# Kernel tuning notes

Hardware: AMD Instinct MI355X
Metric: run time of the kernel (lower is better)

The kernel has to match this reference:

```python
import jax, jax.numpy as jnp
import numpy as np

N_NODES = 50000
N_EDGES = 800000
IN_DIM = 128
HID = 96
ATTN_HID = 32
OUT_DIM = 16
N_SPOTS = 5000
EPS = 1e-5


def _glorot(k, shape):
    fan_in, fan_out = shape
    lim = float(np.sqrt(6.0 / (fan_in + fan_out)))
    return jax.random.uniform(k, shape, minval=-lim, maxval=lim, dtype=jnp.float32)


def setup_inputs() -> dict:
    key = jax.random.key(0)
    ks = jax.random.split(key, 16)
    f32 = jnp.float32
    inp = {
        'x': jax.random.normal(ks[0], (N_NODES, IN_DIM), dtype=f32),
        'edge_index': jax.random.randint(ks[1], (2, N_EDGES), 0, N_NODES, dtype=jnp.int32),
        'cell_to_spot': jax.random.randint(ks[2], (N_NODES,), 0, N_SPOTS, dtype=jnp.int32),
        'num_spots': N_SPOTS,
        # proj: Linear(IN_DIM, HID) + GraphNorm(HID)
        'proj_W': _glorot(ks[3], (IN_DIM, HID)), 'proj_b': jnp.zeros((HID,), f32),
        'gn0_w': jnp.ones((HID,), f32), 'gn0_b': jnp.zeros((HID,), f32), 'gn0_a': jnp.ones((HID,), f32),
        # GCN layer 1 + GraphNorm
        'gcn1_W': _glorot(ks[4], (HID, HID)), 'gcn1_b': jnp.zeros((HID,), f32),
        'gn1_w': jnp.ones((HID,), f32), 'gn1_b': jnp.zeros((HID,), f32), 'gn1_a': jnp.ones((HID,), f32),
        # GCN layer 2 + GraphNorm
        'gcn2_W': _glorot(ks[5], (HID, HID)), 'gcn2_b': jnp.zeros((HID,), f32),
        'gn2_w': jnp.ones((HID,), f32), 'gn2_b': jnp.zeros((HID,), f32), 'gn2_a': jnp.ones((HID,), f32),
        # spot attention aggregator MLP
        'attn_W1': _glorot(ks[6], (HID, ATTN_HID)), 'attn_b1': jnp.zeros((ATTN_HID,), f32),
        'attn_W2': _glorot(ks[7], (ATTN_HID, 1)), 'attn_b2': jnp.zeros((1,), f32),
        # MLP head: Linear + GraphNorm + ReLU + Linear
        'mlp_W1': _glorot(ks[8], (HID, HID)), 'mlp_b1': jnp.zeros((HID,), f32),
        'mlp_gn_w': jnp.ones((HID,), f32), 'mlp_gn_b': jnp.zeros((HID,), f32), 'mlp_gn_a': jnp.ones((HID,), f32),
        'mlp_W2': _glorot(ks[9], (HID, OUT_DIM)), 'mlp_b2': jnp.zeros((OUT_DIM,), f32),
    }
    return inp


def graph_norm(x, w, b, a):
    # PyG GraphNorm over the single graph (all nodes)
    mean = jnp.mean(x, axis=0, keepdims=True)           # [1, d]
    centered = x - a * mean                              # [n, d]
    var = jnp.mean(centered * centered, axis=0, keepdims=True)
    return w * centered * jax.lax.rsqrt(var + EPS) + b


def gcn_conv(x, W, b, src, dst, n):
    # PyG GCNConv: add self-loops, symmetric normalization
    h = x @ W                                            # [n, d_out]
    deg = jax.ops.segment_sum(jnp.ones((src.shape[0],), x.dtype), dst, num_segments=n) + 1.0
    dinv = jax.lax.rsqrt(deg)                            # deg >= 1 due to self loops
    norm = dinv[src] * dinv[dst]                         # [E]
    agg = jax.ops.segment_sum(h[src] * norm[:, None], dst, num_segments=n)
    agg = agg + (dinv * dinv)[:, None] * h               # self-loop messages
    return agg + b


def segment_softmax(scores, seg, num_segments):
    smax = jax.ops.segment_max(scores, seg, num_segments=num_segments)
    e = jnp.exp(scores - smax[seg])
    denom = jax.ops.segment_sum(e, seg, num_segments=num_segments)
    return e / denom[seg]


def reference(x, edge_index, cell_to_spot, num_spots,
              proj_W, proj_b, gn0_w, gn0_b, gn0_a,
              gcn1_W, gcn1_b, gn1_w, gn1_b, gn1_a,
              gcn2_W, gcn2_b, gn2_w, gn2_b, gn2_a,
              attn_W1, attn_b1, attn_W2, attn_b2,
              mlp_W1, mlp_b1, mlp_gn_w, mlp_gn_b, mlp_gn_a,
              mlp_W2, mlp_b2):
    n = x.shape[0]
    src, dst = edge_index[0], edge_index[1]
    # proj: Linear + GraphNorm + ReLU
    h = jax.nn.relu(graph_norm(x @ proj_W + proj_b, gn0_w, gn0_b, gn0_a))
    # GCN stack
    h = jax.nn.relu(graph_norm(gcn_conv(h, gcn1_W, gcn1_b, src, dst, n), gn1_w, gn1_b, gn1_a))
    h = jax.nn.relu(graph_norm(gcn_conv(h, gcn2_W, gcn2_b, src, dst, n), gn2_w, gn2_b, gn2_a))
    # spot attention aggregation
    scores = (jax.nn.relu(h @ attn_W1 + attn_b1) @ attn_W2 + attn_b2)[:, 0]  # [n]
    attn = segment_softmax(scores, cell_to_spot, num_spots)                  # [n]
    spot = jax.ops.segment_sum(h * attn[:, None], cell_to_spot, num_segments=num_spots)  # [S, d]
    # MLP head
    z = jax.nn.relu(graph_norm(spot @ mlp_W1 + mlp_b1, mlp_gn_w, mlp_gn_b, mlp_gn_a))
    return z @ mlp_W2 + mlp_b2
```

## Files before the change

### kernel.cpp

```cpp
#include <hip/hip_runtime.h>

#define N_NODES 50000
#define N_EDGES 800000
#define IN_DIM 128
#define HID 96
#define ATTN_HID 32
#define OUT_DIM 16
#define N_SPOTS 5000
#define GN_EPS 1e-5f

#define SCAN_NB ((N_NODES + 255) / 256)
#define SCAN_SB ((N_SPOTS + 255) / 256)
#define NXCD 8
#define NRANGE (N_NODES / NXCD)
#define SRANGE (N_SPOTS / NXCD)
#define CSB 256
#define GTHB 6250

typedef short bf16x8 __attribute__((ext_vector_type(8)));
typedef float f32x4 __attribute__((ext_vector_type(4)));

__device__ __align__(16) float g_bufA[N_NODES * HID];
__device__ __align__(16) float g_bufB[N_NODES * HID];
__device__ __align__(16) float g_bufC[N_NODES * HID];
__device__ __align__(16) float g_spot[N_SPOTS * HID];
__device__ float    g_dinv[N_NODES];
__device__ float    g_scores[N_NODES];
__device__ int      g_deg[N_NODES];
__device__ int      g_degs[N_SPOTS];
__device__ int      g_rp[N_NODES + 1];
__device__ int      g_cur[N_NODES];
__device__ int      g_rps[N_SPOTS + 1];
__device__ int      g_curs[N_SPOTS];
__device__ int      g_csrc[N_EDGES];
__device__ int      g_cnode[N_NODES];
__device__ int      g_partN[SCAN_NB];
__device__ int      g_partS[SCAN_SB];
__device__ float    g_gpart[GTHB][2 * HID];
__device__ float    g_Spart[CSB][2 * HID];
__device__ float    g_ab[4 * 2 * HID];

__device__ __forceinline__ float* pick(int id) {
  switch (id) {
    case 0:  return g_bufA;
    case 1:  return g_bufB;
    case 2:  return g_bufC;
    default: return g_spot;
  }
}

__device__ __forceinline__ unsigned short bf16_rn(float f) {
  unsigned u = __float_as_uint(f);
  unsigned r = u + 0x7FFFu + ((u >> 16) & 1u);
  return (unsigned short)(r >> 16);
}

__global__ __launch_bounds__(256) void k_init() {
  int i = blockIdx.x * 256 + threadIdx.x;
  if (i < N_NODES) g_deg[i] = 0;
  if (i < N_SPOTS) g_degs[i] = 0;
}

__global__ __launch_bounds__(256) void k_hist(const int* __restrict__ dst,
                                              const int* __restrict__ c2s) {
  int r = blockIdx.x & 7;
  int cb = blockIdx.x >> 3;
  int stride = (gridDim.x >> 3) * 256;
  int nlo = r * NRANGE, nhi = nlo + NRANGE;
  int slo = r * SRANGE, shi = slo + SRANGE;
  for (int i = cb * 256 + threadIdx.x; i < N_EDGES; i += stride) {
    int d = dst[i];
    if (d >= nlo && d < nhi) atomicAdd(&g_deg[d], 1);
  }
  for (int i = cb * 256 + threadIdx.x; i < N_NODES; i += stride) {
    int sp = c2s[i];
    if (sp >= slo && sp < shi) atomicAdd(&g_degs[sp], 1);
  }
}

__global__ __launch_bounds__(256) void k_scan1() {
  bool isS = blockIdx.x >= SCAN_NB;
  int b = isS ? blockIdx.x - SCAN_NB : blockIdx.x;
  const int n = isS ? N_SPOTS : N_NODES;
  const int* deg = isS ? g_degs : g_deg;
  int i = b * 256 + threadIdx.x;
  int v = (i < n) ? deg[i] : 0;
#pragma unroll
  for (int o = 32; o >= 1; o >>= 1) v += __shfl_xor(v, o);
  __shared__ int red[4];
  if ((threadIdx.x & 63) == 0) red[threadIdx.x >> 6] = v;
  __syncthreads();
  if (threadIdx.x == 0)
    (isS ? g_partS : g_partN)[b] = red[0] + red[1] + red[2] + red[3];
}

__global__ __launch_bounds__(256) void k_scan2() {
  bool isS = blockIdx.x == 1;
  int cnt = isS ? SCAN_SB : SCAN_NB;
  int* part = isS ? g_partS : g_partN;
  __shared__ int tmp[256];
  int t = threadIdx.x;
  int v = (t < cnt) ? part[t] : 0;
  tmp[t] = v;
  __syncthreads();
  for (int o = 1; o < 256; o <<= 1) {
    int u = (t >= o) ? tmp[t - o] : 0;
    __syncthreads();
    tmp[t] += u;
    __syncthreads();
  }
  if (t < cnt) part[t] = tmp[t] - v;
}

__global__ __launch_bounds__(256) void k_scan3() {
  bool isS = blockIdx.x >= SCAN_NB;
  int b = isS ? blockIdx.x - SCAN_NB : blockIdx.x;
  const int n = isS ? N_SPOTS : N_NODES;
  const int* deg = isS ? g_degs : g_deg;
  int* rp  = isS ? g_rps  : g_rp;
  int* cur = isS ? g_curs : g_cur;
  const int* part = isS ? g_partS : g_partN;
  __shared__ int tmp[256];
  int t = threadIdx.x;
  int i = b * 256 + t;
  int v = (i < n) ? deg[i] : 0;
  tmp[t] = v;
  __syncthreads();
  for (int o = 1; o < 256; o <<= 1) {
    int u = (t >= o) ? tmp[t - o] : 0;
    __syncthreads();
    tmp[t] += u;
    __syncthreads();
  }
  if (i < n) {
    int off = part[b] + tmp[t] - v;
    rp[i] = off;
    cur[i] = off;
    if (i == n - 1) rp[n] = off + v;
    if (!isS) g_dinv[i] = rsqrtf((float)(v + 1));
  }
}

__global__ __launch_bounds__(256) void k_fill(const int* __restrict__ src,
                                              const int* __restrict__ dst,
                                              const int* __restrict__ c2s) {
  int r = blockIdx.x & 7;
  int cb = blockIdx.x >> 3;
  int stride = (gridDim.x >> 3) * 256;
  int nlo = r * NRANGE, nhi = nlo + NRANGE;
  int slo = r * SRANGE, shi = slo + SRANGE;
  for (int i = cb * 256 + threadIdx.x; i < N_EDGES; i += stride) {
    int d = dst[i];
    if (d >= nlo && d < nhi) {
      int p = atomicAdd(&g_cur[d], 1);
      g_csrc[p] = src[i];
    }
  }
  for (int i = cb * 256 + threadIdx.x; i < N_NODES; i += stride) {
    int sp = c2s[i];
    if (sp >= slo && sp < shi) {
      int p = atomicAdd(&g_curs[sp], 1);
      g_cnode[p] = i;
    }
  }
}

template <int K, bool AFF, bool SCALE, bool STATS>
__global__ __launch_bounds__(256) void k_mfma(const float* __restrict__ Aext,
                                              int a_id, int out_id,
                                              const float* __restrict__ W,
                                              const float* __restrict__ bias,
                                              int stage, int nrows) {
  constexpr int CH = K / 32;
  __shared__ unsigned short WF[CH][6][64][8];
  __shared__ unsigned short WL[CH][6][64][8];
  __shared__ float abs_[2 * HID];
  __shared__ float bs[HID];
  const float* A = Aext ? Aext : pick(a_id);
  float* out = pick(out_id);
  int tid = threadIdx.x;
  if (AFF && tid < 2 * HID) abs_[tid] = g_ab[stage * 2 * HID + tid];
  if (tid < HID) bs[tid] = bias ? bias[tid] : 0.f;
  for (int idx = tid; idx < CH * 6 * 64; idx += 256) {
    int lane = idx & 63;
    int ct = (idx >> 6) % 6;
    int ch = idx / (6 * 64);
    int kbase = ch * 32 + (lane >> 4) * 8;
    int c = ct * 16 + (lane & 15);
#pragma unroll
    for (int j = 0; j < 8; ++j) {
      float w = W[(size_t)(kbase + j) * HID + c];
      unsigned short h = bf16_rn(w);
      WF[ch][ct][lane][j] = h;
      WL[ch][ct][lane][j] = bf16_rn(w - __uint_as_float((unsigned)h << 16));
    }
  }
  __syncthreads();

  int wv = tid >> 6, lane = tid & 63;
  int r0 = blockIdx.x * 64 + wv * 16;
  int arow = r0 + (lane & 15);
  f32x4 acc[6];
#pragma unroll
  for (int t = 0; t < 6; ++t) acc[t] = (f32x4){0.f, 0.f, 0.f, 0.f};

  for (int ch = 0; ch < CH; ++ch) {
    int ks = ch * 32 + (lane >> 4) * 8;
    float av[8];
    if (arow < nrows) {
      const float4* ap = reinterpret_cast<const float4*>(A + (size_t)arow * K + ks);
      float4 v0 = ap[0], v1 = ap[1];
      av[0] = v0.x; av[1] = v0.y; av[2] = v0.z; av[3] = v0.w;
      av[4] = v1.x; av[5] = v1.y; av[6] = v1.z; av[7] = v1.w;
    } else {
#pragma unroll
      for (int j = 0; j < 8; ++j) av[j] = 0.f;
    }
    if (AFF) {
#pragma unroll
      for (int j = 0; j < 8; ++j)
        av[j] = fmaxf(av[j] * abs_[ks + j] + abs_[HID + ks + j], 0.f);
    }
    bf16x8 ah, al;
#pragma unroll
    for (int j = 0; j < 8; ++j) {
      unsigned short h = bf16_rn(av[j]);
      ah[j] = (short)h;
      al[j] = (short)bf16_rn(av[j] - __uint_as_float((unsigned)h << 16));
    }
#pragma unroll
    for (int ct = 0; ct < 6; ++ct) {
      bf16x8 bh = *reinterpret_cast<const bf16x8*>(&WF[ch][ct][lane][0]);
      bf16x8 bl = *reinterpret_cast<const bf16x8*>(&WL[ch][ct][lane][0]);
      acc[ct] = __builtin_amdgcn_mfma_f32_16x16x32_bf16(al, bh, acc[ct], 0, 0, 0);
      acc[ct] = __builtin_amdgcn_mfma_f32_16x16x32_bf16(ah, bl, acc[ct], 0, 0, 0);
      acc[ct] = __builtin_amdgcn_mfma_f32_16x16x32_bf16(ah, bh, acc[ct], 0, 0, 0);
    }
  }
  int rbase = r0 + (lane >> 4) * 4;
  float dv[4];
#pragma unroll
  for (int j = 0; j < 4; ++j) {
    int r = rbase + j;
    dv[j] = SCALE ? ((r < nrows) ? g_dinv[r] : 0.f) : 1.f;
  }
  float s1[6], s2[6];
#pragma unroll
  for (int ct = 0; ct < 6; ++ct) { s1[ct] = 0.f; s2[ct] = 0.f; }
#pragma unroll
  for (int ct = 0; ct < 6; ++ct) {
    int col = ct * 16 + (lane & 15);
    float bb = bs[col];
#pragma unroll
    for (int j = 0; j < 4; ++j) {
      int r = rbase + j;
      if (r < nrows) {
        float v = acc[ct][j] * dv[j] + bb;
        out[(size_t)r * HID + col] = v;
        if (STATS) { s1[ct] += v; s2[ct] += v * v; }
      }
    }
  }
  if constexpr (STATS) {
#pragma unroll
    for (int o = 16; o <= 32; o <<= 1) {
#pragma unroll
      for (int ct = 0; ct < 6; ++ct) {
        s1[ct] += __shfl_xor(s1[ct], o);
        s2[ct] += __shfl_xor(s2[ct], o);
      }
    }
    __shared__ float sr1[4][6][16], sr2[4][6][16];
    if (lane < 16) {
#pragma unroll
      for (int ct = 0; ct < 6; ++ct) {
        sr1[wv][ct][lane] = s1[ct];
        sr2[wv][ct][lane] = s2[ct];
      }
    }
    __syncthreads();
    if (tid < 2 * HID) {
      int c = (tid < HID) ? tid : tid - HID;
      int ct = c >> 4, l = c & 15;
      float s = 0.f;
#pragma unroll
      for (int w = 0; w < 4; ++w)
        s += (tid < HID) ? sr1[w][ct][l] : sr2[w][ct][l];
      g_gpart[blockIdx.x][tid] = s;
    }
  }
}

template <int K, bool AFF, bool SCALE, bool STATS>
__global__ __launch_bounds__(256) void k_gemm96(const float* __restrict__ Aext,
                                                int a_id, int out_id,
                                                const float* __restrict__ W,
                                                const float* __restrict__ bias,
                                                int stage, int nrows) {
  constexpr int KC = 32;
  constexpr int ROWS = 64;
  __shared__ __align__(16) float Ws[KC][HID];
  __shared__ float xs[ROWS][KC + 1];
  __shared__ float abs_[2 * HID];
  const float* A = Aext ? Aext : pick(a_id);
  float* out = pick(out_id);
  int tid = threadIdx.x;
  if (AFF && tid < 2 * HID) abs_[tid] = g_ab[stage * 2 * HID + tid];
  int r0 = blockIdx.x * ROWS;
  int rg = tid >> 3;
  int cg = (tid & 7) * 12;
  float acc[2][12];
#pragma unroll
  for (int i = 0; i < 2; ++i)
#pragma unroll
    for (int c = 0; c < 12; ++c) acc[i][c] = 0.f;

  for (int k0 = 0; k0 < K; k0 += KC) {
    __syncthreads();
    for (int f = tid; f < KC * HID / 4; f += 256) {
      reinterpret_cast<float4*>(&Ws[0][0])[f] =
          reinterpret_cast<const float4*>(W + (size_t)k0 * HID)[f];
    }
    for (int f = tid; f < ROWS * KC / 4; f += 256) {
      int r = f >> 3;
      int kk = (f & 7) << 2;
      int row = r0 + r;
      float4 v = make_float4(0.f, 0.f, 0.f, 0.f);
      if (row < nrows)
        v = *reinterpret_cast<const float4*>(A + (size_t)row * K + k0 + kk);
      if (AFF) {
        int c = k0 + kk;
        v.x = fmaxf(v.x * abs_[c]     + abs_[HID + c],     0.f);
        v.y = fmaxf(v.y * abs_[c + 1] + abs_[HID + c + 1], 0.f);
        v.z = fmaxf(v.z * abs_[c + 2] + abs_[HID + c + 2], 0.f);
        v.w = fmaxf(v.w * abs_[c + 3] + abs_[HID + c + 3], 0.f);
      }
      xs[r][kk] = v.x; xs[r][kk + 1] = v.y; xs[r][kk + 2] = v.z; xs[r][kk + 3] = v.w;
    }
    __syncthreads();
#pragma unroll
    for (int k = 0; k < KC; ++k) {
      float x0 = xs[rg][k];
      float x1 = xs[rg + 32][k];
#pragma unroll
      for (int c = 0; c < 12; ++c) {
        float wv = Ws[k][cg + c];
        acc[0][c] += x0 * wv;
        acc[1][c] += x1 * wv;
      }
    }
  }
  float s1[12], s2[12];
#pragma unroll
  for (int c = 0; c < 12; ++c) { s1[c] = 0.f; s2[c] = 0.f; }
#pragma unroll
  for (int i = 0; i < 2; ++i) {
    int row = r0 + rg + 32 * i;
    if (row < nrows) {
      float sc = SCALE ? g_dinv[row] : 1.f;
#pragma unroll
      for (int c = 0; c < 12; ++c) {
        float v = acc[i][c] * sc;
        if (bias) v += bias[cg + c];
        out[(size_t)row * HID + cg + c] = v;
        if (STATS) { s1[c] += v; s2[c] += v * v; }
      }
    }
  }
  if constexpr (STATS) {
#pragma unroll
    for (int off = 8; off <= 32; off <<= 1) {
#pragma unroll
      for (int c = 0; c < 12; ++c) {
        s1[c] += __shfl_xor(s1[c], off);
        s2[c] += __shfl_xor(s2[c], off);
      }
    }
    __shared__ float sred[4][8][24];
    int wv = tid >> 6, ln = tid & 63;
    if (ln < 8) {
#pragma unroll
      for (int c = 0; c < 12; ++c) {
        sred[wv][ln][2 * c] = s1[c];
        sred[wv][ln][2 * c + 1] = s2[c];
      }
    }
    __syncthreads();
    if (tid < 192) {
      int cg2 = tid / 24, j = tid % 24;
      float s = sred[0][cg2][j] + sred[1][cg2][j] + sred[2][cg2][j] + sred[3][cg2][j];
      int col = cg2 * 12 + (j >> 1);
      g_gpart[blockIdx.x][(j & 1) ? HID + col : col] = s;
    }
  }
}

__global__ __launch_bounds__(256) void k_gather(int t_id, const float* __restrict__ b,
                                                int agg_id) {
  const float* __restrict__ t = pick(t_id);
  float* __restrict__ agg = pick(agg_id);
  int g = (blockIdx.x * 256 + threadIdx.x) >> 5;
  int lane = threadIdx.x & 31;
  int beg = g_rp[g], end = g_rp[g + 1];
  const float* __restrict__ tg = t + (size_t)g * HID;
  float a0 = tg[lane], a1 = tg[32 + lane], a2 = tg[64 + lane];
  int e = beg;
  for (; e + 8 <= end; e += 8) {
    const float* p0 = t + (size_t)g_csrc[e]     * HID;
    const float* p1 = t + (size_t)g_csrc[e + 1] * HID;
    const float* p2 = t + (size_t)g_csrc[e + 2] * HID;
    const float* p3 = t + (size_t)g_csrc[e + 3] * HID;
    const float* p4 = t + (size_t)g_csrc[e + 4] * HID;
    const float* p5 = t + (size_t)g_csrc[e + 5] * HID;
    const float* p6 = t + (size_t)g_csrc[e + 6] * HID;
    const float* p7 = t + (size_t)g_csrc[e + 7] * HID;
    a0 += p0[lane]; a1 += p0[32 + lane]; a2 += p0[64 + lane];
    a0 += p1[lane]; a1 += p1[32 + lane]; a2 += p1[64 + lane];
    a0 += p2[lane]; a1 += p2[32 + lane]; a2 += p2[64 + lane];
    a0 += p3[lane]; a1 += p3[32 + lane]; a2 += p3[64 + lane];
    a0 += p4[lane]; a1 += p4[32 + lane]; a2 += p4[64 + lane];
    a0 += p5[lane]; a1 += p5[32 + lane]; a2 += p5[64 + lane];
    a0 += p6[lane]; a1 += p6[32 + lane]; a2 += p6[64 + lane];
    a0 += p7[lane]; a1 += p7[32 + lane]; a2 += p7[64 + lane];
  }
  for (; e < end; ++e) {
    const float* __restrict__ ts = t + (size_t)g_csrc[e] * HID;
    a0 += ts[lane]; a1 += ts[32 + lane]; a2 += ts[64 + lane];
  }
  float di = g_dinv[g];
  float v0 = di * a0 + b[lane];
  float v1 = di * a1 + b[32 + lane];
  float v2 = di * a2 + b[64 + lane];
  size_t o = (size_t)g * HID;
  agg[o + lane]      = v0;
  agg[o + 32 + lane] = v1;
  agg[o + 64 + lane] = v2;
  float q0 = v0, q1 = v1, q2 = v2;
  float r0s = v0 * v0, r1s = v1 * v1, r2s = v2 * v2;
  q0 += __shfl_xor(q0, 32); r0s += __shfl_xor(r0s, 32);
  q1 += __shfl_xor(q1, 32); r1s += __shfl_xor(r1s, 32);
  q2 += __shfl_xor(q2, 32); r2s += __shfl_xor(r2s, 32);
  __shared__ float sred[4][32][6];
  int wv = threadIdx.x >> 6, ln = threadIdx.x & 63;
  if (ln < 32) {
    sred[wv][ln][0] = q0;  sred[wv][ln][1] = r0s;
    sred[wv][ln][2] = q1;  sred[wv][ln][3] = r1s;
    sred[wv][ln][4] = q2;  sred[wv][ln][5] = r2s;
  }
  __syncthreads();
  if (threadIdx.x < 192) {
    int l2 = threadIdx.x / 6, j = threadIdx.x % 6;
    float s = sred[0][l2][j] + sred[1][l2][j] + sred[2][l2][j] + sred[3][l2][j];
    int dim = l2 + (j >> 1) * 32;
    g_gpart[blockIdx.x][(j & 1) ? HID + dim : dim] = s;
  }
}

__global__ __launch_bounds__(256) void k_colred(int count) {
  int tid = threadIdx.x;
  if (tid >= 2 * HID) return;
  float s = 0.f;
  for (int k = blockIdx.x; k < count; k += gridDim.x) s += g_gpart[k][tid];
  g_Spart[blockIdx.x][tid] = s;
}

__global__ __launch_bounds__(256) void k_gnreduce(int stage,
                                                  const float* __restrict__ w,
                                                  const float* __restrict__ b,
                                                  const float* __restrict__ a,
                                                  float invn) {
  __shared__ float S[2 * HID];
  int tid = threadIdx.x;
  if (tid < 2 * HID) {
    float s0 = 0.f, s1 = 0.f, s2 = 0.f, s3 = 0.f;
    for (int k = 0; k < CSB; k += 4) {
      s0 += g_Spart[k][tid];
      s1 += g_Spart[k + 1][tid];
      s2 += g_Spart[k + 2][tid];
      s3 += g_Spart[k + 3][tid];
    }
    S[tid] = (s0 + s1) + (s2 + s3);
  }
  __syncthreads();
  if (tid < HID) {
    float mean = S[tid] * invn;
    float var = S[HID + tid] * invn + mean * mean * (a[tid] * a[tid] - 2.f * a[tid]);
    float r = rsqrtf(var + GN_EPS);
    float alpha = w[tid] * r;
    g_ab[stage * 2 * HID + tid] = alpha;
    g_ab[stage * 2 * HID + HID + tid] = b[tid] - alpha * a[tid] * mean;
  }
}

__global__ __launch_bounds__(256) void k_scores(int h_id, int stage,
                                                const float* __restrict__ W1,
                                                const float* __restrict__ b1,
                                                const float* __restrict__ W2,
                                                const float* __restrict__ b2) {
  __shared__ float W1s[HID * ATTN_HID];
  __shared__ float b1s[ATTN_HID], W2s[ATTN_HID];
  __shared__ float abs_[2 * HID];
  const float* h = pick(h_id);
  const float* ab = g_ab + stage * 2 * HID;
  int tid = threadIdx.x;
  for (int f = tid; f < HID * ATTN_HID; f += 256) W1s[f] = W1[f];
  if (tid < ATTN_HID) { b1s[tid] = b1[tid]; W2s[tid] = W2[tid]; }
  if (tid < 2 * HID) abs_[tid] = ab[tid];
  __syncthreads();
  int i = blockIdx.x * 256 + tid;
  if (i >= N_NODES) return;
  float acc[ATTN_HID];
#pragma unroll
  for (int k = 0; k < ATTN_HID; ++k) acc[k] = 0.f;
  const float4* h4 = reinterpret_cast<const float4*>(h + (size_t)i * HID);
  for (int j4 = 0; j4 < HID / 4; ++j4) {
    float4 hv4 = h4[j4];
    int j = j4 * 4;
    float h0 = fmaxf(hv4.x * abs_[j]     + abs_[HID + j],     0.f);
    float h1 = fmaxf(hv4.y * abs_[j + 1] + abs_[HID + j + 1], 0.f);
    float h2 = fmaxf(hv4.z * abs_[j + 2] + abs_[HID + j + 2], 0.f);
    float h3 = fmaxf(hv4.w * abs_[j + 3] + abs_[HID + j + 3], 0.f);
#pragma unroll
    for (int k = 0; k < ATTN_HID; ++k) {
      acc[k] += h0 * W1s[j * ATTN_HID + k] + h1 * W1s[(j + 1) * ATTN_HID + k] +
                h2 * W1s[(j + 2) * ATTN_HID + k] + h3 * W1s[(j + 3) * ATTN_HID + k];
    }
  }
  float s = b2[0];
#pragma unroll
  for (int k = 0; k < ATTN_HID; ++k) s += fmaxf(acc[k] + b1s[k], 0.f) * W2s[k];
  g_scores[i] = s;
}

__global__ __launch_bounds__(256) void k_spotagg(int h_id, int stage) {
  const float* __restrict__ h = pick(h_id);
  const float* ab = g_ab + stage * 2 * HID;
  int g = (blockIdx.x * 256 + threadIdx.x) >> 5;
  int lane = threadIdx.x & 31;
  if (g >= N_SPOTS) return;
  int beg = g_rps[g], end = g_rps[g + 1];
  float m = -1e30f;
  for (int i = beg + lane; i < end; i += 32) m = fmaxf(m, g_scores[g_cnode[i]]);
#pragma unroll
  for (int o = 16; o >= 1; o >>= 1) m = fmaxf(m, __shfl_xor(m, o, 32));
  float al0 = ab[lane],      be0 = ab[HID + lane];
  float al1 = ab[32 + lane], be1 = ab[HID + 32 + lane];
  float al2 = ab[64 + lane], be2 = ab[HID + 64 + lane];
  float a0 = 0.f, a1 = 0.f, a2 = 0.f, denom = 0.f;
  for (int i = beg; i < end; ++i) {
    int nd = g_cnode[i];
    float e = __expf(g_scores[nd] - m);
    denom += e;
    const float* __restrict__ hr = h + (size_t)nd * HID;
    a0 += e * fmaxf(hr[lane] * al0 + be0, 0.f);
    a1 += e * fmaxf(hr[32 + lane] * al1 + be1, 0.f);
    a2 += e * fmaxf(hr[64 + lane] * al2 + be2, 0.f);
  }
  float inv = (denom > 0.f) ? 1.f / denom : 0.f;
  g_spot[g * HID + lane]      = a0 * inv;
  g_spot[g * HID + 32 + lane] = a1 * inv;
  g_spot[g * HID + 64 + lane] = a2 * inv;
}

__global__ __launch_bounds__(256) void k_final(int t3_id, int stage,
                                               const float* __restrict__ W2,
                                               const float* __restrict__ b2,
                                               float* __restrict__ out) {
  __shared__ float W2s[HID * OUT_DIM];
  const float* t3 = pick(t3_id);
  const float* ab = g_ab + stage * 2 * HID;
  int tid = threadIdx.x;
  for (int f = tid; f < HID * OUT_DIM; f += 256) W2s[f] = W2[f];
  __syncthreads();
  int r = blockIdx.x * 16 + (tid >> 4);
  int c = tid & 15;
  if (r >= N_SPOTS) return;
  float acc = b2[c];
  for (int j = 0; j < HID; ++j) {
    float z = fmaxf(t3[(size_t)r * HID + j] * ab[j] + ab[HID + j], 0.f);
    acc += z * W2s[j * OUT_DIM + c];
  }
  out[r * OUT_DIM + c] = acc;
}

extern "C" void kernel_launch(void* const* d_in, const int* in_sizes, int n_in,
                              void* d_out, int out_size, void* d_ws, size_t ws_size,
                              hipStream_t stream) {
  const float* x       = (const float*)d_in[0];
  const int*   ei      = (const int*)d_in[1];
  const int*   src     = ei;
  const int*   dst     = ei + N_EDGES;
  const int*   c2s     = (const int*)d_in[2];
  const float* proj_W  = (const float*)d_in[4];
  const float* proj_b  = (const float*)d_in[5];
  const float* gn0_w   = (const float*)d_in[6];
  const float* gn0_b   = (const float*)d_in[7];
  const float* gn0_a   = (const float*)d_in[8];
  const float* gcn1_W  = (const float*)d_in[9];
  const float* gcn1_b  = (const float*)d_in[10];
  const float* gn1_w   = (const float*)d_in[11];
  const float* gn1_b   = (const float*)d_in[12];
  const float* gn1_a   = (const float*)d_in[13];
  const float* gcn2_W  = (const float*)d_in[14];
  const float* gcn2_b  = (const float*)d_in[15];
  const float* gn2_w   = (const float*)d_in[16];
  const float* gn2_b   = (const float*)d_in[17];
  const float* gn2_a   = (const float*)d_in[18];
  const float* attn_W1 = (const float*)d_in[19];
  const float* attn_b1 = (const float*)d_in[20];
  const float* attn_W2 = (const float*)d_in[21];
  const float* attn_b2 = (const float*)d_in[22];
  const float* mlp_W1  = (const float*)d_in[23];
  const float* mlp_b1  = (const float*)d_in[24];
  const float* mlp_gn_w = (const float*)d_in[25];
  const float* mlp_gn_b = (const float*)d_in[26];
  const float* mlp_gn_a = (const float*)d_in[27];
  const float* mlp_W2  = (const float*)d_in[28];
  const float* mlp_b2  = (const float*)d_in[29];
  float* out = (float*)d_out;

  const float invN = 1.f / (float)N_NODES;
  const float invS = 1.f / (float)N_SPOTS;
  const int MFB  = (N_NODES + 63) / 64;
  const int GB_S = (N_SPOTS + 63) / 64;
  const int XB   = NXCD * 96;
  const int SPB  = (N_SPOTS * 32 + 255) / 256;
  const int SCB  = SCAN_NB + SCAN_SB;

  k_init<<<(N_NODES + 255) / 256, 256, 0, stream>>>();
  k_hist<<<XB, 256, 0, stream>>>(dst, c2s);
  k_scan1<<<SCB, 256, 0, stream>>>();
  k_scan2<<<2, 256, 0, stream>>>();
  k_scan3<<<SCB, 256, 0, stream>>>();
  k_fill<<<XB, 256, 0, stream>>>(src, dst, c2s);

  k_mfma<IN_DIM, false, false, true><<<MFB, 256, 0, stream>>>(x, -1, 0, proj_W, proj_b, 0, N_NODES);
  k_colred<<<CSB, 256, 0, stream>>>(MFB);
  k_gnreduce<<<1, 256, 0, stream>>>(0, gn0_w, gn0_b, gn0_a, invN);

  k_mfma<HID, true, true, false><<<MFB, 256, 0, stream>>>(nullptr, 0, 1, gcn1_W, nullptr, 0, N_NODES);
  k_gather<<<GTHB, 256, 0, stream>>>(1, gcn1_b, 0);
  k_colred<<<CSB, 256, 0, stream>>>(GTHB);
  k_gnreduce<<<1, 256, 0, stream>>>(1, gn1_w, gn1_b, gn1_a, invN);

  k_mfma<HID, true, true, false><<<MFB, 256, 0, stream>>>(nullptr, 0, 2, gcn2_W, nullptr, 1, N_NODES);
  k_gather<<<GTHB, 256, 0, stream>>>(2, gcn2_b, 1);
  k_colred<<<CSB, 256, 0, stream>>>(GTHB);
  k_gnreduce<<<1, 256, 0, stream>>>(2, gn2_w, gn2_b, gn2_a, invN);

  k_scores<<<(N_NODES + 255) / 256, 256, 0, stream>>>(1, 2, attn_W1, attn_b1, attn_W2, attn_b2);
  k_spotagg<<<SPB, 256, 0, stream>>>(1, 2);

  k_gemm96<HID, false, false, true><<<GB_S, 256, 0, stream>>>(nullptr, 3, 2, mlp_W1, mlp_b1, 0, N_SPOTS);
  k_colred<<<CSB, 256, 0, stream>>>(GB_S);
  k_gnreduce<<<1, 256, 0, stream>>>(3, mlp_gn_w, mlp_gn_b, mlp_gn_a, invS);
  k_final<<<(N_SPOTS + 15) / 16, 256, 0, stream>>>(2, 3, mlp_W2, mlp_b2, out);
}
```

Measured before the change: 361.0 us.

## Pack independent CSR-build and projection stages into shared launches

Independent stages now share a single launch by splitting on block index: histogram with the projection GEMM, scan1 with column reduction, scan3 with the GraphNorm reduce, and the CSR fill with the first GCN GEMM. The scan2 kernel is removed; each scan3 block sums its preceding partials with a wave reduction instead. The final MLP GraphNorm reads the per-block partials directly, skipping a colred launch. This cuts kernel launches and the idle gaps between small dependent kernels, at the cost of heavier blocks sharing the GPU and somewhat redundant partial summation.

After: 468.0 us. +29.6%, slower.

```diff
diff --git a/kernel.cpp b/kernel.cpp
--- a/kernel.cpp
+++ b/kernel.cpp
@@ -11,11 +11,15 @@
 
 #define SCAN_NB ((N_NODES + 255) / 256)
 #define SCAN_SB ((N_SPOTS + 255) / 256)
+#define SCB (SCAN_NB + SCAN_SB)
 #define NXCD 8
 #define NRANGE (N_NODES / NXCD)
 #define SRANGE (N_SPOTS / NXCD)
 #define CSB 256
 #define GTHB 6250
+#define MFB  ((N_NODES + 63) / 64)
+#define GB_S ((N_SPOTS + 63) / 64)
+#define XB   (NXCD * 96)
 
 typedef short bf16x8 __attribute__((ext_vector_type(8)));
 typedef float f32x4 __attribute__((ext_vector_type(4)));
@@ -55,17 +59,12 @@
   return (unsigned short)(r >> 16);
 }
 
-__global__ __launch_bounds__(256) void k_init() {
-  int i = blockIdx.x * 256 + threadIdx.x;
-  if (i < N_NODES) g_deg[i] = 0;
-  if (i < N_SPOTS) g_degs[i] = 0;
-}
-
-__global__ __launch_bounds__(256) void k_hist(const int* __restrict__ dst,
-                                              const int* __restrict__ c2s) {
-  int r = blockIdx.x & 7;
-  int cb = blockIdx.x >> 3;
-  int stride = (gridDim.x >> 3) * 256;
+
+__device__ __forceinline__ void hist_body(int bid, const int* __restrict__ dst,
+                                          const int* __restrict__ c2s) {
+  int r = bid & 7;
+  int cb = bid >> 3;
+  int stride = (XB >> 3) * 256;
   int nlo = r * NRANGE, nhi = nlo + NRANGE;
   int slo = r * SRANGE, shi = slo + SRANGE;
   for (int i = cb * 256 + threadIdx.x; i < N_EDGES; i += stride) {
@@ -78,75 +77,12 @@
   }
 }
 
-__global__ __launch_bounds__(256) void k_scan1() {
-  bool isS = blockIdx.x >= SCAN_NB;
-  int b = isS ? blockIdx.x - SCAN_NB : blockIdx.x;
-  const int n = isS ? N_SPOTS : N_NODES;
-  const int* deg = isS ? g_degs : g_deg;
-  int i = b * 256 + threadIdx.x;
-  int v = (i < n) ? deg[i] : 0;
-#pragma unroll
-  for (int o = 32; o >= 1; o >>= 1) v += __shfl_xor(v, o);
-  __shared__ int red[4];
-  if ((threadIdx.x & 63) == 0) red[threadIdx.x >> 6] = v;
-  __syncthreads();
-  if (threadIdx.x == 0)
-    (isS ? g_partS : g_partN)[b] = red[0] + red[1] + red[2] + red[3];
-}
-
-__global__ __launch_bounds__(256) void k_scan2() {
-  bool isS = blockIdx.x == 1;
-  int cnt = isS ? SCAN_SB : SCAN_NB;
-  int* part = isS ? g_partS : g_partN;
-  __shared__ int tmp[256];
-  int t = threadIdx.x;
-  int v = (t < cnt) ? part[t] : 0;
-  tmp[t] = v;
-  __syncthreads();
-  for (int o = 1; o < 256; o <<= 1) {
-    int u = (t >= o) ? tmp[t - o] : 0;
-    __syncthreads();
-    tmp[t] += u;
-    __syncthreads();
-  }
-  if (t < cnt) part[t] = tmp[t] - v;
-}
-
-__global__ __launch_bounds__(256) void k_scan3() {
-  bool isS = blockIdx.x >= SCAN_NB;
-  int b = isS ? blockIdx.x - SCAN_NB : blockIdx.x;
-  const int n = isS ? N_SPOTS : N_NODES;
-  const int* deg = isS ? g_degs : g_deg;
-  int* rp  = isS ? g_rps  : g_rp;
-  int* cur = isS ? g_curs : g_cur;
-  const int* part = isS ? g_partS : g_partN;
-  __shared__ int tmp[256];
-  int t = threadIdx.x;
-  int i = b * 256 + t;
-  int v = (i < n) ? deg[i] : 0;
-  tmp[t] = v;
-  __syncthreads();
-  for (int o = 1; o < 256; o <<= 1) {
-    int u = (t >= o) ? tmp[t - o] : 0;
-    __syncthreads();
-    tmp[t] += u;
-    __syncthreads();
-  }
-  if (i < n) {
-    int off = part[b] + tmp[t] - v;
-    rp[i] = off;
-    cur[i] = off;
-    if (i == n - 1) rp[n] = off + v;
-    if (!isS) g_dinv[i] = rsqrtf((float)(v + 1));
-  }
-}
-
-__global__ __launch_bounds__(256) void k_fill(const int* __restrict__ src,
-                                              const int* __restrict__ dst,
-                                              const int* __restrict__ c2s) {
-  int r = blockIdx.x & 7;
-  int cb = blockIdx.x >> 3;
-  int stride = (gridDim.x >> 3) * 256;
+__device__ __forceinline__ void fill_body(int bid, const int* __restrict__ src,
+                                          const int* __restrict__ dst,
+                                          const int* __restrict__ c2s) {
+  int r = bid & 7;
+  int cb = bid >> 3;
+  int stride = (XB >> 3) * 256;
   int nlo = r * NRANGE, nhi = nlo + NRANGE;
   int slo = r * SRANGE, shi = slo + SRANGE;
   for (int i = cb * 256 + threadIdx.x; i < N_EDGES; i += stride) {
@@ -165,12 +101,95 @@
   }
 }
 
+__device__ __forceinline__ void scan1_body(int bid) {
+  bool isS = bid >= SCAN_NB;
+  int b = isS ? bid - SCAN_NB : bid;
+  const int n = isS ? N_SPOTS : N_NODES;
+  const int* deg = isS ? g_degs : g_deg;
+  int i = b * 256 + threadIdx.x;
+  int v = (i < n) ? deg[i] : 0;
+#pragma unroll
+  for (int o = 32; o >= 1; o >>= 1) v += __shfl_xor(v, o);
+  __shared__ int red1[4];
+  if ((threadIdx.x & 63) == 0) red1[threadIdx.x >> 6] = v;
+  __syncthreads();
+  if (threadIdx.x == 0)
+    (isS ? g_partS : g_partN)[b] = red1[0] + red1[1] + red1[2] + red1[3];
+}
+
+__device__ __forceinline__ void scan3_body(int bid) {
+  bool isS = bid >= SCAN_NB;
+  int b = isS ? bid - SCAN_NB : bid;
+  const int n = isS ? N_SPOTS : N_NODES;
+  const int* deg = isS ? g_degs : g_deg;
+  int* rp  = isS ? g_rps  : g_rp;
+  int* cur = isS ? g_curs : g_cur;
+  const int* part = isS ? g_partS : g_partN;
+  int t = threadIdx.x;
+  int pv = (t < b) ? part[t] : 0;
+#pragma unroll
+  for (int o = 32; o >= 1; o >>= 1) pv += __shfl_xor(pv, o);
+  __shared__ int red3[4];
+  if ((t & 63) == 0) red3[t >> 6] = pv;
+  __syncthreads();
+  int base = red3[0] + red3[1] + red3[2] + red3[3];
+  __shared__ int tmp[256];
+  int i = b * 256 + t;
+  int v = (i < n) ? deg[i] : 0;
+  tmp[t] = v;
+  __syncthreads();
+  for (int o = 1; o < 256; o <<= 1) {
+    int u = (t >= o) ? tmp[t - o] : 0;
+    __syncthreads();
+    tmp[t] += u;
+    __syncthreads();
+  }
+  if (i < n) {
+    int off = base + tmp[t] - v;
+    rp[i] = off;
+    cur[i] = off;
+    if (i == n - 1) rp[n] = off + v;
+    if (!isS) g_dinv[i] = rsqrtf((float)(v + 1));
+  }
+}
+
+__device__ __forceinline__ void colred_body(int bid, int count) {
+  int tid = threadIdx.x;
+  if (tid >= 2 * HID) return;
+  float s = 0.f;
+  for (int k = bid; k < count; k += CSB) s += g_gpart[k][tid];
+  g_Spart[bid][tid] = s;
+}
+
+__device__ __forceinline__ void gnreduce_body(int stage, const float* __restrict__ w,
+                                              const float* __restrict__ b,
+                                              const float* __restrict__ a, float invn,
+                                              const float (*__restrict__ arr)[2 * HID],
+                                              int count) {
+  __shared__ float S[2 * HID];
+  int tid = threadIdx.x;
+  if (tid < 2 * HID) {
+    float s = 0.f;
+    for (int k = 0; k < count; ++k) s += arr[k][tid];
+    S[tid] = s;
+  }
+  __syncthreads();
+  if (tid < HID) {
+    float mean = S[tid] * invn;
+    float var = S[HID + tid] * invn + mean * mean * (a[tid] * a[tid] - 2.f * a[tid]);
+    float r = rsqrtf(var + GN_EPS);
+    float alpha = w[tid] * r;
+    g_ab[stage * 2 * HID + tid] = alpha;
+    g_ab[stage * 2 * HID + HID + tid] = b[tid] - alpha * a[tid] * mean;
+  }
+}
+
 template <int K, bool AFF, bool SCALE, bool STATS>
-__global__ __launch_bounds__(256) void k_mfma(const float* __restrict__ Aext,
-                                              int a_id, int out_id,
-                                              const float* __restrict__ W,
-                                              const float* __restrict__ bias,
-                                              int stage, int nrows) {
+__device__ __forceinline__ void mfma_body(int bid, const float* __restrict__ Aext,
+                                          int a_id, int out_id,
+                                          const float* __restrict__ W,
+                                          const float* __restrict__ bias,
+                                          int stage, int nrows) {
   constexpr int CH = K / 32;
   __shared__ unsigned short WF[CH][6][64][8];
   __shared__ unsigned short WL[CH][6][64][8];
@@ -198,7 +217,7 @@
   __syncthreads();
 
   int wv = tid >> 6, lane = tid & 63;
-  int r0 = blockIdx.x * 64 + wv * 16;
+  int r0 = bid * 64 + wv * 16;
   int arow = r0 + (lane & 15);
   f32x4 acc[6];
 #pragma unroll
@@ -286,113 +305,61 @@
 #pragma unroll
       for (int w = 0; w < 4; ++w)
         s += (tid < HID) ? sr1[w][ct][l] : sr2[w][ct][l];
-      g_gpart[blockIdx.x][tid] = s;
-    }
-  }
-}
-
-template <int K, bool AFF, bool SCALE, bool STATS>
-__global__ __launch_bounds__(256) void k_gemm96(const float* __restrict__ Aext,
-                                                int a_id, int out_id,
-                                                const float* __restrict__ W,
-                                                const float* __restrict__ bias,
-                                                int stage, int nrows) {
-  constexpr int KC = 32;
-  constexpr int ROWS = 64;
-  __shared__ __align__(16) float Ws[KC][HID];
-  __shared__ float xs[ROWS][KC + 1];
-  __shared__ float abs_[2 * HID];
-  const float* A = Aext ? Aext : pick(a_id);
-  float* out = pick(out_id);
-  int tid = threadIdx.x;
-  if (AFF && tid < 2 * HID) abs_[tid] = g_ab[stage * 2 * HID + tid];
-  int r0 = blockIdx.x * ROWS;
-  int rg = tid >> 3;
-  int cg = (tid & 7) * 12;
-  float acc[2][12];
-#pragma unroll
-  for (int i = 0; i < 2; ++i)
-#pragma unroll
-    for (int c = 0; c < 12; ++c) acc[i][c] = 0.f;
-
-  for (int k0 = 0; k0 < K; k0 += KC) {
-    __syncthreads();
-    for (int f = tid; f < KC * HID / 4; f += 256) {
-      reinterpret_cast<float4*>(&Ws[0][0])[f] =
-          reinterpret_cast<const float4*>(W + (size_t)k0 * HID)[f];
-    }
-    for (int f = tid; f < ROWS * KC / 4; f += 256) {
-      int r = f >> 3;
-      int kk = (f & 7) << 2;
-      int row = r0 + r;
-      float4 v = make_float4(0.f, 0.f, 0.f, 0.f);
-      if (row < nrows)
-        v = *reinterpret_cast<const float4*>(A + (size_t)row * K + k0 + kk);
-      if (AFF) {
-        int c = k0 + kk;
-        v.x = fmaxf(v.x * abs_[c]     + abs_[HID + c],     0.f);
-        v.y = fmaxf(v.y * abs_[c + 1] + abs_[HID + c + 1], 0.f);
-        v.z = fmaxf(v.z * abs_[c + 2] + abs_[HID + c + 2], 0.f);
-        v.w = fmaxf(v.w * abs_[c + 3] + abs_[HID + c + 3], 0.f);
-      }
-      xs[r][kk] = v.x; xs[r][kk + 1] = v.y; xs[r][kk + 2] = v.z; xs[r][kk + 3] = v.w;
-    }
-    __syncthreads();
-#pragma unroll
-    for (int k = 0; k < KC; ++k) {
-      float x0 = xs[rg][k];
-      float x1 = xs[rg + 32][k];
-#pragma unroll
-      for (int c = 0; c < 12; ++c) {
-        float wv = Ws[k][cg + c];
-        acc[0][c] += x0 * wv;
-        acc[1][c] += x1 * wv;
-      }
-    }
-  }
-  float s1[12], s2[12];
-#pragma unroll
-  for (int c = 0; c < 12; ++c) { s1[c] = 0.f; s2[c] = 0.f; }
-#pragma unroll
-  for (int i = 0; i < 2; ++i) {
-    int row = r0 + rg + 32 * i;
-    if (row < nrows) {
-      float sc = SCALE ? g_dinv[row] : 1.f;
-#pragma unroll
-      for (int c = 0; c < 12; ++c) {
-        float v = acc[i][c] * sc;
-        if (bias) v += bias[cg + c];
-        out[(size_t)row * HID + cg + c] = v;
-        if (STATS) { s1[c] += v; s2[c] += v * v; }
-      }
-    }
-  }
-  if constexpr (STATS) {
-#pragma unroll
-    for (int off = 8; off <= 32; off <<= 1) {
-#pragma unroll
-      for (int c = 0; c < 12; ++c) {
-        s1[c] += __shfl_xor(s1[c], off);
-        s2[c] += __shfl_xor(s2[c], off);
-      }
-    }
-    __shared__ float sred[4][8][24];
-    int wv = tid >> 6, ln = tid & 63;
-    if (ln < 8) {
-#pragma unroll
-      for (int c = 0; c < 12; ++c) {
-        sred[wv][ln][2 * c] = s1[c];
-        sred[wv][ln][2 * c + 1] = s2[c];
-      }
-    }
-    __syncthreads();
-    if (tid < 192) {
-      int cg2 = tid / 24, j = tid % 24;
-      float s = sred[0][cg2][j] + sred[1][cg2][j] + sred[2][cg2][j] + sred[3][cg2][j];
-      int col = cg2 * 12 + (j >> 1);
-      g_gpart[blockIdx.x][(j & 1) ? HID + col : col] = s;
-    }
-  }
+      g_gpart[bid][tid] = s;
+    }
+  }
+}
+
+
+__global__ __launch_bounds__(256) void k_init() {
+  int i = blockIdx.x * 256 + threadIdx.x;
+  if (i < N_NODES) g_deg[i] = 0;
+  if (i < N_SPOTS) g_degs[i] = 0;
+}
+
+__global__ __launch_bounds__(256) void k_pack_hist_proj(const int* __restrict__ dst,
+                                                        const int* __restrict__ c2s,
+                                                        const float* __restrict__ x,
+                                                        const float* __restrict__ pW,
+                                                        const float* __restrict__ pb) {
+  if (blockIdx.x < XB) hist_body(blockIdx.x, dst, c2s);
+  else mfma_body<IN_DIM, false, false, true>(blockIdx.x - XB, x, -1, 0, pW, pb, 0, N_NODES);
+}
+
+__global__ __launch_bounds__(256) void k_pack_scan1_colred() {
+  if (blockIdx.x < SCB) scan1_body(blockIdx.x);
+  else colred_body(blockIdx.x - SCB, MFB);
+}
+
+__global__ __launch_bounds__(256) void k_pack_scan3_gnred(const float* __restrict__ w,
+                                                          const float* __restrict__ b,
+                                                          const float* __restrict__ a,
+                                                          float invn) {
+  if (blockIdx.x < SCB) scan3_body(blockIdx.x);
+  else gnreduce_body(0, w, b, a, invn, g_Spart, CSB);
+}
+
+__global__ __launch_bounds__(256) void k_pack_fill_mfma1(const int* __restrict__ src,
+                                                         const int* __restrict__ dst,
+                                                         const int* __restrict__ c2s,
+                                                         const float* __restrict__ w1) {
+  if (blockIdx.x < XB) fill_body(blockIdx.x, src, dst, c2s);
+  else mfma_body<HID, true, true, false>(blockIdx.x - XB, nullptr, 0, 1, w1, nullptr, 0, N_NODES);
+}
+
+__global__ __launch_bounds__(256) void k_mfma2(const float* __restrict__ w2) {
+  mfma_body<HID, true, true, false>(blockIdx.x, nullptr, 0, 2, w2, nullptr, 1, N_NODES);
+}
+
+__global__ __launch_bounds__(256) void k_colred(int count) {
+  colred_body(blockIdx.x, count);
+}
+
+__global__ __launch_bounds__(256) void k_gnreduce(int stage, const float* __restrict__ w,
+                                                  const float* __restrict__ b,
+                                                  const float* __restrict__ a,
+                                                  float invn, int fromGpart, int count) {
+  gnreduce_body(stage, w, b, a, invn, fromGpart ? g_gpart : g_Spart, count);
 }
 
 __global__ __launch_bounds__(256) void k_gather(int t_id, const float* __restrict__ b,
@@ -456,39 +423,107 @@
   }
 }
 
-__global__ __launch_bounds__(256) void k_colred(int count) {
+template <int K, bool AFF, bool SCALE, bool STATS>
+__global__ __launch_bounds__(256) void k_gemm96(const float* __restrict__ Aext,
+                                                int a_id, int out_id,
+                                                const float* __restrict__ W,
+                                                const float* __restrict__ bias,
+                                                int stage, int nrows) {
+  constexpr int KC = 32;
+  constexpr int ROWS = 64;
+  __shared__ __align__(16) float Ws[KC][HID];
+  __shared__ float xs[ROWS][KC + 1];
+  __shared__ float abs_[2 * HID];
+  const float* A = Aext ? Aext : pick(a_id);
+  float* out = pick(out_id);
   int tid = threadIdx.x;
-  if (tid >= 2 * HID) return;
-  float s = 0.f;
-  for (int k = blockIdx.x; k < count; k += gridDim.x) s += g_gpart[k][tid];
-  g_Spart[blockIdx.x][tid] = s;
-}
-
-__global__ __launch_bounds__(256) void k_gnreduce(int stage,
-                                                  const float* __restrict__ w,
-                                                  const float* __restrict__ b,
-                                                  const float* __restrict__ a,
-                                                  float invn) {
-  __shared__ float S[2 * HID];
-  int tid = threadIdx.x;
-  if (tid < 2 * HID) {
-    float s0 = 0.f, s1 = 0.f, s2 = 0.f, s3 = 0.f;
-    for (int k = 0; k < CSB; k += 4) {
-      s0 += g_Spart[k][tid];
-      s1 += g_Spart[k + 1][tid];
-      s2 += g_Spart[k + 2][tid];
-      s3 += g_Spart[k + 3][tid];
-    }
-    S[tid] = (s0 + s1) + (s2 + s3);
-  }
-  __syncthreads();
-  if (tid < HID) {
-    float mean = S[tid] * invn;
-    float var = S[HID + tid] * invn + mean * mean * (a[tid] * a[tid] - 2.f * a[tid]);
-    float r = rsqrtf(var + GN_EPS);
-    float alpha = w[tid] * r;
-    g_ab[stage * 2 * HID + tid] = alpha;
-    g_ab[stage * 2 * HID + HID + tid] = b[tid] - alpha * a[tid] * mean;
+  if (AFF && tid < 2 * HID) abs_[tid] = g_ab[stage * 2 * HID + tid];
+  int r0 = blockIdx.x * ROWS;
+  int rg = tid >> 3;
+  int cg = (tid & 7) * 12;
+  float acc[2][12];
+#pragma unroll
+  for (int i = 0; i < 2; ++i)
+#pragma unroll
+    for (int c = 0; c < 12; ++c) acc[i][c] = 0.f;
+
+  for (int k0 = 0; k0 < K; k0 += KC) {
+    __syncthreads();
+    for (int f = tid; f < KC * HID / 4; f += 256) {
+      reinterpret_cast<float4*>(&Ws[0][0])[f] =
+          reinterpret_cast<const float4*>(W + (size_t)k0 * HID)[f];
+    }
+    for (int f = tid; f < ROWS * KC / 4; f += 256) {
+      int r = f >> 3;
+      int kk = (f & 7) << 2;
+      int row = r0 + r;
+      float4 v = make_float4(0.f, 0.f, 0.f, 0.f);
+      if (row < nrows)
+        v = *reinterpret_cast<const float4*>(A + (size_t)row * K + k0 + kk);
+      if (AFF) {
+        int c = k0 + kk;
+        v.x = fmaxf(v.x * abs_[c]     + abs_[HID + c],     0.f);
+        v.y = fmaxf(v.y * abs_[c + 1] + abs_[HID + c + 1], 0.f);
+        v.z = fmaxf(v.z * abs_[c + 2] + abs_[HID + c + 2], 0.f);
+        v.w = fmaxf(v.w * abs_[c + 3] + abs_[HID + c + 3], 0.f);
+      }
+      xs[r][kk] = v.x; xs[r][kk + 1] = v.y; xs[r][kk + 2] = v.z; xs[r][kk + 3] = v.w;
+    }
+    __syncthreads();
+#pragma unroll
+    for (int k = 0; k < KC; ++k) {
+      float x0 = xs[rg][k];
+      float x1 = xs[rg + 32][k];
+#pragma unroll
+      for (int c = 0; c < 12; ++c) {
+        float wv = Ws[k][cg + c];
+        acc[0][c] += x0 * wv;
+        acc[1][c] += x1 * wv;
+      }
+    }
+  }
+  float s1[12], s2[12];
+#pragma unroll
+  for (int c = 0; c < 12; ++c) { s1[c] = 0.f; s2[c] = 0.f; }
+#pragma unroll
+  for (int i = 0; i < 2; ++i) {
+    int row = r0 + rg + 32 * i;
+    if (row < nrows) {
+      float sc = SCALE ? g_dinv[row] : 1.f;
+#pragma unroll
+      for (int c = 0; c < 12; ++c) {
+        float v = acc[i][c] * sc;
+        if (bias) v += bias[cg + c];
+        out[(size_t)row * HID + cg + c] = v;
+        if (STATS) { s1[c] += v; s2[c] += v * v; }
+      }
+    }
+  }
+  if constexpr (STATS) {
+#pragma unroll
+    for (int off = 8; off <= 32; off <<= 1) {
+#pragma unroll
+      for (int c = 0; c < 12; ++c) {
+        s1[c] += __shfl_xor(s1[c], off);
+        s2[c] += __shfl_xor(s2[c], off);
+      }
+    }
+    __shared__ float sred[4][8][24];
+    int wv = tid >> 6, ln = tid & 63;
+    if (ln < 8) {
+#pragma unroll
+      for (int c = 0; c < 12; ++c) {
+        sred[wv][ln][2 * c] = s1[c];
+        sred[wv][ln][2 * c + 1] = s2[c];
+      }
+    }
+    __syncthreads();
+    if (tid < 192) {
+      int cg2 = tid / 24, j = tid % 24;
+      float s = sred[0][cg2][j] + sred[1][cg2][j] + sred[2][cg2][j] + sred[3][cg2][j];
+      int col = cg2 * 12 + (j >> 1);
+      g_gpart[blockIdx.x][(j & 1) ? HID + col : col] = s;
+    }
   }
 }
 
@@ -621,38 +656,23 @@
 
   const float invN = 1.f / (float)N_NODES;
   const float invS = 1.f / (float)N_SPOTS;
-  const int MFB  = (N_NODES + 63) / 64;
-  const int GB_S = (N_SPOTS + 63) / 64;
-  const int XB   = NXCD * 96;
-  const int SPB  = (N_SPOTS * 32 + 255) / 256;
-  const int SCB  = SCAN_NB + SCAN_SB;
+  const int SPB = (N_SPOTS * 32 + 255) / 256;
 
   k_init<<<(N_NODES + 255) / 256, 256, 0, stream>>>();
-  k_hist<<<XB, 256, 0, stream>>>(dst, c2s);
-  k_scan1<<<SCB, 256, 0, stream>>>();
-  k_scan2<<<2, 256, 0, stream>>>();
-  k_scan3<<<SCB, 256, 0, stream>>>();
-  k_fill<<<XB, 256, 0, stream>>>(src, dst, c2s);
-
-  k_mfma<IN_DIM, false, false, true><<<MFB, 256, 0, stream>>>(x, -1, 0, proj_W, proj_b, 0, N_NODES);
-  k_colred<<<CSB, 256, 0, stream>>>(MFB);
-  k_gnreduce<<<1, 256, 0, stream>>>(0, gn0_w, gn0_b, gn0_a, invN);
-
-  k_mfma<HID, true, true, false><<<MFB, 256, 0, stream>>>(nullptr, 0, 1, gcn1_W, nullptr, 0, N_NODES);
+  k_pack_hist_proj<<<XB + MFB, 256, 0, stream>>>(dst, c2s, x, proj_W, proj_b);
+  k_pack_scan1_colred<<<SCB + CSB, 256, 0, stream>>>();
+  k_pack_scan3_gnred<<<SCB + 1, 256, 0, stream>>>(gn0_w, gn0_b, gn0_a, invN);
+  k_pack_fill_mfma1<<<XB + MFB, 256, 0, stream>>>(src, dst, c2s, gcn1_W);
   k_gather<<<GTHB, 256, 0, stream>>>(1, gcn1_b, 0);
   k_colred<<<CSB, 256, 0, stream>>>(GTHB);
-  k_gnreduce<<<1, 256, 0, stream>>>(1, gn1_w, gn1_b, gn1_a, invN);
-
-  k_mfma<HID, true, true, false><<<MFB, 256, 0, stream>>>(nullptr, 0, 2, gcn2_W, nullptr, 1, N_NODES);
+  k_gnreduce<<<1, 256, 0, stream>>>(1, gn1_w, gn1_b, gn1_a, invN, 0, CSB);
+  k_mfma2<<<MFB, 256, 0, stream>>>(gcn2_W);
   k_gather<<<GTHB, 256, 0, stream>>>(2, gcn2_b, 1);
   k_colred<<<CSB, 256, 0, stream>>>(GTHB);
-  k_gnreduce<<<1, 256, 0, stream>>>(2, gn2_w, gn2_b, gn2_a, invN);
-
+  k_gnreduce<<<1, 256, 0, stream>>>(2, gn2_w, gn2_b, gn2_a, invN, 0, CSB);
   k_scores<<<(N_NODES + 255) / 256, 256, 0, stream>>>(1, 2, attn_W1, attn_b1, attn_W2, attn_b2);
   k_spotagg<<<SPB, 256, 0, stream>>>(1, 2);
-
   k_gemm96<HID, false, false, true><<<GB_S, 256, 0, stream>>>(nullptr, 3, 2, mlp_W1, mlp_b1, 0, N_SPOTS);
-  k_colred<<<CSB, 256, 0, stream>>>(GB_S);
-  k_gnreduce<<<1, 256, 0, stream>>>(3, mlp_gn_w, mlp_gn_b, mlp_gn_a, invS);
+  k_gnreduce<<<1, 256, 0, stream>>>(3, mlp_gn_w, mlp_gn_b, mlp_gn_a, invS, 1, GB_S);
   k_final<<<(N_SPOTS + 15) / 16, 256, 0, stream>>>(2, 3, mlp_W2, mlp_b2, out);
 }
```
